# Kernel tuning notes

Hardware: AMD Instinct MI355X
Metric: run time of the kernel (lower is better)

## Reference

```python
import jax, jax.numpy as jnp
import numpy as np

D = 16          # manifold_dim
M = 8192        # mem_slots
H = 256         # slot_dim
K_BASE = 32     # topk
K_BIG = 48      # int(K_BASE * 1.5), used when internal lightbulb fires
INPUT_DIM = 1024
ODE_HID = 128
ODE_STEPS = 2
ODE_DT = 0.5
TEMPERATURE = 1.0      # buffer initial value
LB_TOP1_AVG = 1.0      # buffer initial value
LB_DROP_RATIO = 0.7
BIG = 1e30


def layer_norm(x, g, b, eps=1e-5):
    mu = jnp.mean(x, axis=-1, keepdims=True)
    var = jnp.mean(jnp.square(x - mu), axis=-1, keepdims=True)
    return (x - mu) * jax.lax.rsqrt(var + eps) * g + b


def setup_inputs() -> dict:
    key = jax.random.key(0)
    ks = jax.random.split(key, 12)
    B, S = 4, 2048
    T3 = D * 3
    s_in = 1.0 / np.sqrt(INPUT_DIM)
    s_3d = 1.0 / np.sqrt(T3)
    s_h = 1.0 / np.sqrt(H)
    s_ode = 1.0 / np.sqrt(ODE_HID)
    return {
        "x": jax.random.normal(ks[0], (B, S, INPUT_DIM), jnp.float32),
        "W_proj": jax.random.normal(ks[1], (INPUT_DIM, T3), jnp.float32) * s_in,
        "b_proj": jnp.zeros((T3,), jnp.float32),
        "ln1_g": jnp.ones((T3,), jnp.float32),
        "ln1_b": jnp.zeros((T3,), jnp.float32),
        "ode_W1": jax.random.normal(ks[2], (T3, ODE_HID), jnp.float32) * s_3d,
        "ode_b1": jnp.zeros((ODE_HID,), jnp.float32),
        "ode_W2": jax.random.normal(ks[3], (ODE_HID, T3), jnp.float32) * s_ode,
        "ode_b2": jnp.zeros((T3,), jnp.float32),
        "memory_slots": jax.random.normal(ks[4], (M, H), jnp.float32),
        "pos_enc": jax.random.normal(ks[5], (M, D, 3), jnp.float32),
        "curvature": jax.random.normal(ks[6], (M, D), jnp.float32),
        "curv_alpha": jnp.float32(0.1),
        "W_out": jax.random.normal(ks[7], (H, INPUT_DIM), jnp.float32) * s_h,
        "b_out": jnp.zeros((INPUT_DIM,), jnp.float32),
        "ln2_g": jnp.ones((INPUT_DIM,), jnp.float32),
        "ln2_b": jnp.zeros((INPUT_DIM,), jnp.float32),
    }


def reference(x, W_proj, b_proj, ln1_g, ln1_b, ode_W1, ode_b1, ode_W2, ode_b2,
              memory_slots, pos_enc, curvature, curv_alpha, W_out, b_out, ln2_g, ln2_b):
    # manifold projection: Linear -> LayerNorm -> GELU   (B,S,3D)
    h = jax.nn.gelu(layer_norm(x @ W_proj + b_proj, ln1_g, ln1_b), approximate=False)
    # ODE evolution (2 steps): x + dt * MLP(x), operating on flattened (B,S,3D)
    for _ in range(ODE_STEPS):
        dh = jnp.tanh(h @ ode_W1 + ode_b1) @ ode_W2 + ode_b2
        h = h + ODE_DT * dh
    # _attend: query positions are detached in the original
    q = jax.lax.stop_gradient(h)                       # (B,S,3D)
    mem_pos = pos_enc.reshape(M, D * 3)                # (M,3D)
    # fast pairwise squared-L2 distance: ||q||^2 + ||m||^2 - 2 q.m
    q2 = jnp.sum(q * q, axis=-1, keepdims=True)        # (B,S,1)
    m2 = jnp.sum(mem_pos * mem_pos, axis=-1)           # (M,)
    dist = jnp.maximum(q2 + m2 - 2.0 * jnp.einsum('bsd,md->bsm', q, mem_pos), 0.0)
    dist = dist / max(TEMPERATURE, 1e-6)
    curv_w = jnp.exp(-curv_alpha * jnp.linalg.norm(curvature, axis=-1))  # (M,)
    dist = dist * curv_w                               # (B,S,M)
    # dynamic top-K: take K_BIG smallest, mask down to K_BASE if lightbulb not fired
    neg_vals, itop = jax.lax.top_k(-dist, K_BIG)       # smallest K_BIG distances
    dtop = -neg_vals                                    # ascending (B,S,K_BIG)
    top1 = jnp.mean(dtop[..., 0])
    internal_fire = top1 < LB_DROP_RATIO * LB_TOP1_AVG
    keep = jnp.logical_or(internal_fire, jnp.arange(K_BIG) < K_BASE)  # (K_BIG,)
    d_eff = jnp.where(keep, dtop, BIG)
    w = jax.nn.softmax(-d_eff, axis=-1)                # (B,S,K_BIG)
    mem = memory_slots[itop]                           # gather (B,S,K_BIG,H)
    attended = jnp.einsum('bsk,bskh->bsh', w, mem)     # (B,S,H)
    out = jax.nn.gelu(layer_norm(attended @ W_out + b_out, ln2_g, ln2_b), approximate=False)
    return out
```

## Files before the change

### kernel.cpp

```cpp
#include <hip/hip_runtime.h>
#include <math.h>

#define NQ    8192
#define T3    48
#define INDIM 1024
#define HID   128
#define MSLOT 8192
#define HD    256
#define KBIG  48
#define KBASE 32
#define NSAMP 1024
#define CAP   1024
#define MAXB  32

#define OFF_QH    ((size_t)0)
#define OFF_QL    ((size_t)1048576)
#define OFF_Q2    ((size_t)2097152)
#define OFF_M2    ((size_t)2129920)
#define OFF_CW    ((size_t)2162688)
#define OFF_TOPV  ((size_t)2195456)
#define OFF_TOPI  ((size_t)3768320)
#define OFF_RMIN  ((size_t)5341184)
#define OFF_FLAG  ((size_t)5373952)
#define OFF_WOT   ((size_t)5374208)
#define OFF_PEH   ((size_t)5898496)
#define OFF_PEL   ((size_t)6947072)
#define OFF_WPTH  ((size_t)7995648)
#define OFF_WPTL  ((size_t)8093952)
#define OFF_H0    ((size_t)8192256)
#define OFF_RTHR  ((size_t)9765120)
#define OFF_CNT   ((size_t)9797888)
#define OFF_ATTB  ((size_t)9830656)
#define OFF_DISTS ((size_t)14024960)
#define OFF_CANDS ((size_t)47579392)

typedef __attribute__((ext_vector_type(8))) short short8;
typedef __attribute__((ext_vector_type(4))) float f32x4;

__device__ __forceinline__ float gelu_exact(float x) {
    return 0.5f * x * (1.0f + erff(x * 0.70710678118654752f));
}

__device__ __forceinline__ unsigned short bf16_rne(float f) {
    unsigned int x = __float_as_uint(f);
    unsigned int r = (x + 0x7fffu + ((x >> 16) & 1u)) >> 16;
    return (unsigned short)r;
}

__device__ __forceinline__ void split2(float x, unsigned short& h, unsigned short& l) {
    h = bf16_rne(x);
    l = bf16_rne(x - __uint_as_float((unsigned)h << 16));
}

__global__ __launch_bounds__(256) void k0_prep(const float* __restrict__ pe,
        const float* __restrict__ curv, const float* __restrict__ alpha,
        float* __restrict__ m2, float* __restrict__ cw,
        unsigned short* __restrict__ ph, unsigned short* __restrict__ pl) {
    int m = blockIdx.x * 256 + threadIdx.x;
    float s = 0.f;
    for (int d = 0; d < T3; d++) { float v = pe[(size_t)m * T3 + d]; s += v * v; }
    m2[m] = s;
    float c = 0.f;
    for (int d = 0; d < 16; d++) { float v = curv[m * 16 + d]; c += v * v; }
    cw[m] = expf(-alpha[0] * sqrtf(c));
    int base = blockIdx.x * 256;
    for (int idx = threadIdx.x; idx < 256 * 64; idx += 256) {
        int r = idx >> 6, cc = idx & 63;
        unsigned short hi = 0, lo = 0;
        if (cc < T3) split2(pe[(size_t)(base + r) * T3 + cc], hi, lo);
        size_t o = (size_t)(base + r) * 64 + cc;
        ph[o] = hi; pl[o] = lo;
    }
}

__global__ __launch_bounds__(256) void k0b_cvt(const float* __restrict__ Wo,
        unsigned short* __restrict__ Wot) {
    __shared__ float t[64][65];
    int k0 = blockIdx.x * 64;
    int n0 = blockIdx.y * 64;
    int c = threadIdx.x & 63, r4 = threadIdx.x >> 6;
    #pragma unroll
    for (int i = 0; i < 16; i++) {
        int kr = i * 4 + r4;
        t[kr][c] = Wo[(size_t)(k0 + kr) * INDIM + n0 + c];
    }
    __syncthreads();
    #pragma unroll
    for (int i = 0; i < 16; i++) {
        int nr = i * 4 + r4;
        Wot[(size_t)(n0 + nr) * HD + k0 + c] = bf16_rne(t[c][nr]);
    }
}

__global__ __launch_bounds__(256) void k0d_wpt(const float* __restrict__ Wp,
        unsigned short* __restrict__ wph, unsigned short* __restrict__ wpl) {
    int n = blockIdx.x;
    for (int k = threadIdx.x; k < INDIM; k += 256) {
        unsigned short h, l;
        split2(Wp[(size_t)k * T3 + n], h, l);
        wph[(size_t)n * INDIM + k] = h;
        wpl[(size_t)n * INDIM + k] = l;
    }
}

__global__ __launch_bounds__(256) void k1_mfma(const float* __restrict__ x,
        const unsigned short* __restrict__ wph, const unsigned short* __restrict__ wpl,
        float* __restrict__ h0) {
    __shared__ float part[4][16][48];
    int tid = threadIdx.x, lane = tid & 63, wv = tid >> 6;
    int r0 = blockIdx.x * 16;
    int lm = lane & 15, lk8 = (lane >> 4) * 8;
    f32x4 acc[3];
    #pragma unroll
    for (int j = 0; j < 3; j++) acc[j] = (f32x4)(0.f);
    int kw = wv * 256;
    for (int ks = 0; ks < 8; ks++) {
        int kofs = kw + ks * 32 + lk8;
        short8 ah, al, bh[3], bl[3];
        {
            const float* xp = x + (size_t)(r0 + lm) * INDIM + kofs;
            float4 xa = *(const float4*)xp;
            float4 xb = *(const float4*)(xp + 4);
            float va[8] = {xa.x, xa.y, xa.z, xa.w, xb.x, xb.y, xb.z, xb.w};
            #pragma unroll
            for (int e = 0; e < 8; e++) {
                unsigned short h, l;
                split2(va[e], h, l);
                ah[e] = (short)h; al[e] = (short)l;
            }
        }
        #pragma unroll
        for (int j = 0; j < 3; j++) {
            size_t bo = (size_t)(j * 16 + lm) * INDIM + kofs;
            bh[j] = *(const short8*)(wph + bo);
            bl[j] = *(const short8*)(wpl + bo);
        }
        #pragma unroll
        for (int j = 0; j < 3; j++) {
            f32x4 a = acc[j];
            a = __builtin_amdgcn_mfma_f32_16x16x32_bf16(ah, bh[j], a, 0, 0, 0);
            a = __builtin_amdgcn_mfma_f32_16x16x32_bf16(ah, bl[j], a, 0, 0, 0);
            a = __builtin_amdgcn_mfma_f32_16x16x32_bf16(al, bh[j], a, 0, 0, 0);
            acc[j] = a;
        }
    }
    int orow = (lane >> 4) * 4;
    #pragma unroll
    for (int j = 0; j < 3; j++)
        #pragma unroll
        for (int r = 0; r < 4; r++)
            part[wv][orow + r][j * 16 + lm] = acc[j][r];
    __syncthreads();
    for (int idx = tid; idx < 16 * 48; idx += 256) {
        int rr = idx / 48, cc = idx - rr * 48;
        float s = part[0][rr][cc] + part[1][rr][cc] + part[2][rr][cc] + part[3][rr][cc];
        h0[(size_t)(r0 + rr) * T3 + cc] = s;
    }
}

__global__ __launch_bounds__(256) void k1b_ode(const float* __restrict__ h0,
        const float* __restrict__ bp,
        const float* __restrict__ g1, const float* __restrict__ b1ln,
        const float* __restrict__ W1, const float* __restrict__ bb1,
        const float* __restrict__ W2, const float* __restrict__ bb2,
        unsigned short* __restrict__ qh, unsigned short* __restrict__ ql,
        float* __restrict__ q2out) {
    __shared__ __align__(16) float W1s[T3 * HID];
    __shared__ __align__(16) float W2s[HID * T3];
    __shared__ __align__(16) float hs[16 * T3];
    __shared__ __align__(16) float t1s[16 * 132];
    int tid = threadIdx.x;
    size_t base = (size_t)blockIdx.x * 16 * T3;
    for (int i = tid; i < 1536; i += 256) {
        *(float4*)&W1s[i * 4] = *(const float4*)&W1[i * 4];
        *(float4*)&W2s[i * 4] = *(const float4*)&W2[i * 4];
    }
    for (int idx = tid; idx < 16 * T3; idx += 256) {
        int c = idx % T3;
        t1s[idx] = bp[c] + h0[base + idx];
    }
    __syncthreads();
    {
        int r = tid >> 4, c16 = tid & 15;
        float v[3];
        float ssum = 0.f;
        #pragma unroll
        for (int i = 0; i < 3; i++) { v[i] = t1s[r * T3 + c16 * 3 + i]; ssum += v[i]; }
        #pragma unroll
        for (int off = 1; off < 16; off <<= 1) ssum += __shfl_xor(ssum, off);
        float mean = ssum * (1.f / T3);
        float vv = 0.f;
        #pragma unroll
        for (int i = 0; i < 3; i++) { v[i] -= mean; vv += v[i] * v[i]; }
        #pragma unroll
        for (int off = 1; off < 16; off <<= 1) vv += __shfl_xor(vv, off);
        float rstd = rsqrtf(vv * (1.f / T3) + 1e-5f);
        #pragma unroll
        for (int i = 0; i < 3; i++) {
            int c = c16 * 3 + i;
            hs[r * T3 + c] = gelu_exact(v[i] * rstd * g1[c] + b1ln[c]);
        }
    }
    __syncthreads();
    for (int step = 0; step < 2; step++) {
        #pragma unroll
        for (int it = 0; it < 2; it++) {
            int idx = tid + it * 256;
            int rr = idx >> 5, j4 = idx & 31;
            float4 a = *(const float4*)&bb1[j4 * 4];
            #pragma unroll 3
            for (int d4 = 0; d4 < 12; d4++) {
                float4 qv = *(const float4*)&hs[rr * T3 + d4 * 4];
                float qa[4] = {qv.x, qv.y, qv.z, qv.w};
                #pragma unroll
                for (int dd = 0; dd < 4; dd++) {
                    float4 wv = *(const float4*)&W1s[(d4 * 4 + dd) * HID + j4 * 4];
                    a.x += qa[dd] * wv.x; a.y += qa[dd] * wv.y;
                    a.z += qa[dd] * wv.z; a.w += qa[dd] * wv.w;
                }
            }
            a.x = tanhf(a.x); a.y = tanhf(a.y); a.z = tanhf(a.z); a.w = tanhf(a.w);
            *(float4*)&t1s[rr * 132 + j4 * 4] = a;
        }
        __syncthreads();
        if (tid < 192) {
            int rr = tid / 12, c4 = tid % 12;
            float4 a = *(const float4*)&bb2[c4 * 4];
            #pragma unroll 4
            for (int j4 = 0; j4 < 32; j4++) {
                float4 tv = *(const float4*)&t1s[rr * 132 + j4 * 4];
                float ta[4] = {tv.x, tv.y, tv.z, tv.w};
                #pragma unroll
                for (int jj = 0; jj < 4; jj++) {
                    float4 wv = *(const float4*)&W2s[(j4 * 4 + jj) * T3 + c4 * 4];
                    a.x += ta[jj] * wv.x; a.y += ta[jj] * wv.y;
                    a.z += ta[jj] * wv.z; a.w += ta[jj] * wv.w;
                }
            }
            float4 cur = *(const float4*)&hs[rr * T3 + c4 * 4];
            cur.x += 0.5f * a.x; cur.y += 0.5f * a.y;
            cur.z += 0.5f * a.z; cur.w += 0.5f * a.w;
            *(float4*)&hs[rr * T3 + c4 * 4] = cur;
        }
        __syncthreads();
    }
    {
        int r = tid >> 4, c16 = tid & 15;
        float sq = 0.f;
        #pragma unroll
        for (int i = 0; i < 3; i++) { float v = hs[r * T3 + c16 * 3 + i]; sq += v * v; }
        #pragma unroll
        for (int off = 1; off < 16; off <<= 1) sq += __shfl_xor(sq, off);
        if (c16 == 0) q2out[(size_t)blockIdx.x * 16 + r] = sq;
    }
    for (int idx = tid; idx < 16 * 64; idx += 256) {
        int r = idx >> 6, c = idx & 63;
        unsigned short hi = 0, lo = 0;
        if (c < T3) split2(hs[r * T3 + c], hi, lo);
        size_t o = ((size_t)blockIdx.x * 16 + r) * 64 + c;
        qh[o] = hi; ql[o] = lo;
    }
}

#define PES 72
__global__ __launch_bounds__(256, 4) void k2a_mfma(
        const unsigned short* __restrict__ qh, const unsigned short* __restrict__ ql,
        const float* __restrict__ q2g,
        const unsigned short* __restrict__ ph, const unsigned short* __restrict__ pl,
        const float* __restrict__ m2, const float* __restrict__ cw,
        float* __restrict__ dist, int rowstride) {
    __shared__ __align__(16) char smem[256 * PES * 2];
    __shared__ float q2s[32];
    unsigned short* pesh = (unsigned short*)smem;
    int tid = threadIdx.x, lane = tid & 63, wv = tid >> 6;
    int c0 = blockIdx.x * 256;
    int grow0 = blockIdx.y * 32;
    for (int idx = tid; idx < 2048; idx += 256) {
        int col = idx >> 3, ch = idx & 7;
        *(uint4*)&pesh[col * PES + ch * 8] = *(const uint4*)&ph[(size_t)(c0 + col) * 64 + ch * 8];
    }
    if (tid < 32) q2s[tid] = q2g[grow0 + tid];
    int lm = lane & 15, lk8 = (lane >> 4) * 8;
    int mco = wv * 64;
    short8 bqh[2][2], bql[2][2];
    #pragma unroll
    for (int qs = 0; qs < 2; qs++)
        #pragma unroll
        for (int ks = 0; ks < 2; ks++) {
            size_t o = (size_t)(grow0 + qs * 16 + lm) * 64 + ks * 32 + lk8;
            bqh[qs][ks] = *(const short8*)&qh[o];
            bql[qs][ks] = *(const short8*)&ql[o];
        }
    short8 al0[4], al1[4];
    #pragma unroll
    for (int ms = 0; ms < 4; ms++) {
        size_t plo = (size_t)(c0 + mco + ms * 16 + lm) * 64;
        al0[ms] = *(const short8*)&pl[plo + lk8];
        al1[ms] = *(const short8*)&pl[plo + 32 + lk8];
    }
    __syncthreads();
    f32x4 acc[4][2];
    #pragma unroll
    for (int i = 0; i < 4; i++)
        #pragma unroll
        for (int j = 0; j < 2; j++) acc[i][j] = (f32x4)(0.f);
    #pragma unroll
    for (int ms = 0; ms < 4; ms++) {
        int arow = mco + ms * 16 + lm;
        short8 ah0 = *(const short8*)&pesh[arow * PES + lk8];
        short8 ah1 = *(const short8*)&pesh[arow * PES + 32 + lk8];
        #pragma unroll
        for (int qs = 0; qs < 2; qs++) {
            f32x4 a = acc[ms][qs];
            a = __builtin_amdgcn_mfma_f32_16x16x32_bf16(ah0, bqh[qs][0], a, 0, 0, 0);
            a = __builtin_amdgcn_mfma_f32_16x16x32_bf16(ah1, bqh[qs][1], a, 0, 0, 0);
            a = __builtin_amdgcn_mfma_f32_16x16x32_bf16(ah0, bql[qs][0], a, 0, 0, 0);
            a = __builtin_amdgcn_mfma_f32_16x16x32_bf16(ah1, bql[qs][1], a, 0, 0, 0);
            a = __builtin_amdgcn_mfma_f32_16x16x32_bf16(al0[ms], bqh[qs][0], a, 0, 0, 0);
            a = __builtin_amdgcn_mfma_f32_16x16x32_bf16(al1[ms], bqh[qs][1], a, 0, 0, 0);
            acc[ms][qs] = a;
        }
    }
    int mr4 = (lane >> 4) * 4;
    #pragma unroll
    for (int ms = 0; ms < 4; ms++) {
        int gm = c0 + mco + ms * 16 + mr4;
        float4 m2v = *(const float4*)&m2[gm];
        float4 cwv = *(const float4*)&cw[gm];
        float m2a[4] = {m2v.x, m2v.y, m2v.z, m2v.w};
        float cwa[4] = {cwv.x, cwv.y, cwv.z, cwv.w};
        #pragma unroll
        for (int qs = 0; qs < 2; qs++) {
            float q2 = q2s[qs * 16 + lm];
            #pragma unroll
            for (int c = 0; c < 4; c++)
                acc[ms][qs][c] = fmaxf(q2 + m2a[c] - 2.f * acc[ms][qs][c], 0.f) * cwa[c];
        }
    }
    __syncthreads();
    float (*dt)[260] = (float(*)[260])smem;
    #pragma unroll
    for (int ms = 0; ms < 4; ms++)
        #pragma unroll
        for (int qs = 0; qs < 2; qs++) {
            float4 o;
            o.x = acc[ms][qs][0]; o.y = acc[ms][qs][1];
            o.z = acc[ms][qs][2]; o.w = acc[ms][qs][3];
            *(float4*)&dt[qs * 16 + lm][mco + ms * 16 + mr4] = o;
        }
    __syncthreads();
    #pragma unroll
    for (int i = 0; i < 8; i++) {
        int qrow = wv * 8 + i;
        float4 v = *(const float4*)&dt[qrow][lane * 4];
        *(float4*)&dist[(size_t)(grow0 + qrow) * rowstride + c0 + lane * 4] = v;
    }
}

#define NBINT 2048
#define MAXCT 512
__global__ __launch_bounds__(256) void k2b_thr(const float* __restrict__ dists,
        float* __restrict__ rowthr, int* __restrict__ cnt) {
    __shared__ unsigned int hist[NBINT];
    __shared__ unsigned long long cand[MAXCT];
    __shared__ float s_wmin[4], s_wmax[4];
    __shared__ unsigned int wsum[4];
    __shared__ unsigned int s_B, s_ncand;
    int tid = threadIdx.x, lane = tid & 63, wv = tid >> 6;
    int row = blockIdx.x;
    float4 v4 = *(const float4*)(dists + (size_t)row * NSAMP + tid * 4);
    float fv[4] = {v4.x, v4.y, v4.z, v4.w};
    float mn = fminf(fminf(fv[0], fv[1]), fminf(fv[2], fv[3]));
    float mx = fmaxf(fmaxf(fv[0], fv[1]), fmaxf(fv[2], fv[3]));
    #pragma unroll
    for (int off = 32; off; off >>= 1) {
        mn = fminf(mn, __shfl_xor(mn, off));
        mx = fmaxf(mx, __shfl_xor(mx, off));
    }
    if (lane == 0) { s_wmin[wv] = mn; s_wmax[wv] = mx; }
    __syncthreads();
    float m0 = fminf(fminf(s_wmin[0], s_wmin[1]), fminf(s_wmin[2], s_wmin[3]));
    float mX = fmaxf(fmaxf(s_wmax[0], s_wmax[1]), fmaxf(s_wmax[2], s_wmax[3]));
    float lo = m0;
    float width = fmaxf(m0 * 0.5f, 1e-3f);
    float fullw = fmaxf((mX - m0) * 1.0001f, 1e-3f) + 1e-6f;
    unsigned B = 0;
    float scale = 0.f, hiT = 0.f;
    for (int att = 0; att < 7; att++) {
        if (att == 6 || width > fullw) width = fullw;
        hiT = lo + width;
        scale = (float)NBINT / width;
        for (int i = tid; i < NBINT; i += 256) hist[i] = 0;
        __syncthreads();
        #pragma unroll
        for (int j = 0; j < 4; j++) {
            float v = fv[j];
            if (v < hiT) {
                int b = (int)((v - lo) * scale);
                b = b < NBINT - 1 ? b : NBINT - 1;
                atomicAdd(&hist[b], 1u);
            }
        }
        __syncthreads();
        unsigned hb[8];
        unsigned s = 0;
        #pragma unroll
        for (int i = 0; i < 8; i++) { hb[i] = hist[tid * 8 + i]; s += hb[i]; }
        unsigned v = s;
        #pragma unroll
        for (int off = 1; off < 64; off <<= 1) {
            unsigned o = __shfl_up(v, off);
            if (lane >= off) v += o;
        }
        if (lane == 63) wsum[wv] = v;
        __syncthreads();
        unsigned wbase = 0;
        for (int w = 0; w < wv; w++) wbase += wsum[w];
        unsigned total = wsum[0] + wsum[1] + wsum[2] + wsum[3];
        if (total >= KBIG) {
            unsigned excl = wbase + v - s;
            if (excl < KBIG && KBIG <= excl + s) {
                unsigned c = excl;
                #pragma unroll
                for (int i = 0; i < 8; i++) {
                    if (c < KBIG && KBIG <= c + hb[i]) { s_B = tid * 8 + i; break; }
                    c += hb[i];
                }
            }
            __syncthreads();
            B = s_B;
            break;
        }
        width *= 8.f;
        __syncthreads();
    }
    if (tid == 0) s_ncand = 0;
    __syncthreads();
    #pragma unroll
    for (int j = 0; j < 4; j++) {
        float v = fv[j];
        if (v < hiT) {
            int b = (int)((v - lo) * scale);
            b = b < NBINT - 1 ? b : NBINT - 1;
            if ((unsigned)b <= B) {
                unsigned n = atomicAdd(&s_ncand, 1u);
                if (n < MAXCT)
                    cand[n] = ((unsigned long long)__float_as_uint(v) << 32)
                              | (unsigned)(tid * 4 + j);
            }
        }
    }
    __syncthreads();
    int nc = (int)(s_ncand < MAXCT ? s_ncand : MAXCT);
    for (int i = tid; i < nc; i += 256) {
        unsigned long long me = cand[i];
        int rank = 0;
        for (int j = 0; j < nc; j++) rank += (cand[j] < me) ? 1 : 0;
        if (rank == KBIG - 1)
            rowthr[row] = __uint_as_float((unsigned)(me >> 32));
    }
    if (tid == 0) cnt[row] = 0;
}

__global__ __launch_bounds__(256, 4) void k2c_filter(
        const unsigned short* __restrict__ qh, const unsigned short* __restrict__ ql,
        const float* __restrict__ q2g,
        const unsigned short* __restrict__ ph, const unsigned short* __restrict__ pl,
        const float* __restrict__ m2, const float* __restrict__ cw,
        const float* __restrict__ rowthr, int* __restrict__ cnt,
        unsigned long long* __restrict__ cands) {
    __shared__ __align__(16) char smem[256 * PES * 2];
    __shared__ float q2s[32];
    __shared__ float thrs[32];
    __shared__ unsigned int lcnt[32], gbase[32];
    unsigned short* pesh = (unsigned short*)smem;
    int tid = threadIdx.x, lane = tid & 63, wv = tid >> 6;
    int c0 = blockIdx.x * 256;
    int grow0 = blockIdx.y * 32;
    for (int idx = tid; idx < 2048; idx += 256) {
        int col = idx >> 3, ch = idx & 7;
        *(uint4*)&pesh[col * PES + ch * 8] = *(const uint4*)&ph[(size_t)(c0 + col) * 64 + ch * 8];
    }
    if (tid < 32) {
        q2s[tid] = q2g[grow0 + tid];
        thrs[tid] = rowthr[grow0 + tid];
        lcnt[tid] = 0;
    }
    int lm = lane & 15, lk8 = (lane >> 4) * 8;
    int mco = wv * 64;
    short8 bqh[2][2], bql[2][2];
    #pragma unroll
    for (int qs = 0; qs < 2; qs++)
        #pragma unroll
        for (int ks = 0; ks < 2; ks++) {
            size_t o = (size_t)(grow0 + qs * 16 + lm) * 64 + ks * 32 + lk8;
            bqh[qs][ks] = *(const short8*)&qh[o];
            bql[qs][ks] = *(const short8*)&ql[o];
        }
    short8 al0[4], al1[4];
    #pragma unroll
    for (int ms = 0; ms < 4; ms++) {
        size_t plo = (size_t)(c0 + mco + ms * 16 + lm) * 64;
        al0[ms] = *(const short8*)&pl[plo + lk8];
        al1[ms] = *(const short8*)&pl[plo + 32 + lk8];
    }
    __syncthreads();
    f32x4 acc[4][2];
    #pragma unroll
    for (int i = 0; i < 4; i++)
        #pragma unroll
        for (int j = 0; j < 2; j++) acc[i][j] = (f32x4)(0.f);
    #pragma unroll
    for (int ms = 0; ms < 4; ms++) {
        int arow = mco + ms * 16 + lm;
        short8 ah0 = *(const short8*)&pesh[arow * PES + lk8];
        short8 ah1 = *(const short8*)&pesh[arow * PES + 32 + lk8];
        #pragma unroll
        for (int qs = 0; qs < 2; qs++) {
            f32x4 a = acc[ms][qs];
            a = __builtin_amdgcn_mfma_f32_16x16x32_bf16(ah0, bqh[qs][0], a, 0, 0, 0);
            a = __builtin_amdgcn_mfma_f32_16x16x32_bf16(ah1, bqh[qs][1], a, 0, 0, 0);
            a = __builtin_amdgcn_mfma_f32_16x16x32_bf16(ah0, bql[qs][0], a, 0, 0, 0);
            a = __builtin_amdgcn_mfma_f32_16x16x32_bf16(ah1, bql[qs][1], a, 0, 0, 0);
            a = __builtin_amdgcn_mfma_f32_16x16x32_bf16(al0[ms], bqh[qs][0], a, 0, 0, 0);
            a = __builtin_amdgcn_mfma_f32_16x16x32_bf16(al1[ms], bqh[qs][1], a, 0, 0, 0);
            acc[ms][qs] = a;
        }
    }
    int mr4 = (lane >> 4) * 4;
    #pragma unroll
    for (int ms = 0; ms < 4; ms++) {
        int gm = c0 + mco + ms * 16 + mr4;
        float4 m2v = *(const float4*)&m2[gm];
        float4 cwv = *(const float4*)&cw[gm];
        float m2a[4] = {m2v.x, m2v.y, m2v.z, m2v.w};
        float cwa[4] = {cwv.x, cwv.y, cwv.z, cwv.w};
        #pragma unroll
        for (int qs = 0; qs < 2; qs++) {
            float q2 = q2s[qs * 16 + lm];
            #pragma unroll
            for (int c = 0; c < 4; c++)
                acc[ms][qs][c] = fmaxf(q2 + m2a[c] - 2.f * acc[ms][qs][c], 0.f) * cwa[c];
        }
    }
    __syncthreads();
    unsigned long long (*lbuf)[MAXB] = (unsigned long long(*)[MAXB])smem;
    #pragma unroll
    for (int ms = 0; ms < 4; ms++) {
        int gm = c0 + mco + ms * 16 + mr4;
        #pragma unroll
        for (int qs = 0; qs < 2; qs++) {
            int q = qs * 16 + lm;
            float thr = thrs[q];
            #pragma unroll
            for (int c = 0; c < 4; c++) {
                float v = acc[ms][qs][c];
                if (v <= thr) {
                    unsigned long long key =
                        ((unsigned long long)__float_as_uint(v) << 32)
                        | (unsigned)(gm + c);
                    unsigned slot = atomicAdd(&lcnt[q], 1u);
                    if (slot < MAXB) lbuf[q][slot] = key;
                    else {
                        int gs = atomicAdd(&cnt[grow0 + q], 1);
                        if (gs < CAP) cands[(size_t)(grow0 + q) * CAP + gs] = key;
                    }
                }
            }
        }
    }
    __syncthreads();
    if (tid < 32) {
        unsigned k = lcnt[tid];
        k = k < MAXB ? k : MAXB;
        lcnt[tid] = k;
        gbase[tid] = (unsigned)atomicAdd(&cnt[grow0 + tid], (int)k);
    }
    __syncthreads();
    for (int idx = tid; idx < 32 * MAXB; idx += 256) {
        int q = idx >> 5, i = idx & (MAXB - 1);
        if (i < (int)lcnt[q]) {
            unsigned b = gbase[q] + (unsigned)i;
            if (b < CAP) cands[(size_t)(grow0 + q) * CAP + b] = lbuf[q][i];
        }
    }
}

#define NBIND 2048
#define FINCAP 512
__global__ __launch_bounds__(256) void k2d_select(
        const unsigned long long* __restrict__ cands, const int* __restrict__ cnt,
        float* __restrict__ topv, int* __restrict__ topi, float* __restrict__ rowmin) {
    __shared__ unsigned long long cl[CAP];
    __shared__ unsigned int hist[NBIND];
    __shared__ unsigned long long fin[FINCAP];
    __shared__ float s_mn[4], s_mx[4];
    __shared__ unsigned int wsum[4];
    __shared__ unsigned int s_B, s_nfin;
    int tid = threadIdx.x, lane = tid & 63, wv = tid >> 6;
    size_t row = blockIdx.x;
    int nc = cnt[row];
    nc = nc < CAP ? nc : CAP;
    float mn = 3.4e38f, mx = -3.4e38f;
    for (int i = tid; i < nc; i += 256) {
        unsigned long long k = cands[row * CAP + i];
        cl[i] = k;
        float v = __uint_as_float((unsigned)(k >> 32));
        mn = fminf(mn, v); mx = fmaxf(mx, v);
    }
    #pragma unroll
    for (int off = 32; off; off >>= 1) {
        mn = fminf(mn, __shfl_xor(mn, off));
        mx = fmaxf(mx, __shfl_xor(mx, off));
    }
    if (lane == 0) { s_mn[wv] = mn; s_mx[wv] = mx; }
    for (int i = tid; i < NBIND; i += 256) hist[i] = 0;
    if (tid == 0) s_nfin = 0;
    __syncthreads();
    float m0 = fminf(fminf(s_mn[0], s_mn[1]), fminf(s_mn[2], s_mn[3]));
    float mX = fmaxf(fmaxf(s_mx[0], s_mx[1]), fmaxf(s_mx[2], s_mx[3]));
    float width = fmaxf((mX - m0) * 1.0001f, 1e-9f) + 1e-12f;
    float scale = (float)NBIND / width;
    for (int i = tid; i < nc; i += 256) {
        float v = __uint_as_float((unsigned)(cl[i] >> 32));
        int b = (int)((v - m0) * scale);
        b = b < NBIND - 1 ? b : NBIND - 1;
        atomicAdd(&hist[b], 1u);
    }
    __syncthreads();
    {
        unsigned hb[8];
        unsigned s = 0;
        #pragma unroll
        for (int i = 0; i < 8; i++) { hb[i] = hist[tid * 8 + i]; s += hb[i]; }
        unsigned v = s;
        #pragma unroll
        for (int off = 1; off < 64; off <<= 1) {
            unsigned o = __shfl_up(v, off);
            if (lane >= off) v += o;
        }
        if (lane == 63) wsum[wv] = v;
        __syncthreads();
        unsigned wbase = 0;
        for (int w = 0; w < wv; w++) wbase += wsum[w];
        unsigned excl = wbase + v - s;
        unsigned tgt = (unsigned)(nc < KBIG ? nc : KBIG);
        if (excl < tgt && tgt <= excl + s) {
            unsigned c = excl;
            #pragma unroll
            for (int i = 0; i < 8; i++) {
                if (c < tgt && tgt <= c + hb[i]) { s_B = tid * 8 + i; break; }
                c += hb[i];
            }
        }
        __syncthreads();
    }
    unsigned B = s_B;
    for (int i = tid; i < nc; i += 256) {
        float v = __uint_as_float((unsigned)(cl[i] >> 32));
        int b = (int)((v - m0) * scale);
        b = b < NBIND - 1 ? b : NBIND - 1;
        if ((unsigned)b <= B) {
            unsigned n = atomicAdd(&s_nfin, 1u);
            if (n < FINCAP) fin[n] = cl[i];
        }
    }
    __syncthreads();
    int nf = (int)s_nfin;
    if (nf <= FINCAP) {
        for (int i = tid; i < nf; i += 256) {
            unsigned long long me = fin[i];
            int rank = 0;
            for (int j = 0; j < nf; j++) rank += (fin[j] < me) ? 1 : 0;
            if (rank < KBIG) {
                float v = __uint_as_float((unsigned)(me >> 32));
                topv[row * KBIG + rank] = v;
                topi[row * KBIG + rank] = (int)(me & 0xFFFFFFFFu);
                if (rank == 0) rowmin[row] = v;
            }
        }
    } else {
        for (int i = tid; i < nc; i += 256) {
            unsigned long long me = cl[i];
            int rank = 0;
            for (int j = 0; j < nc; j++) rank += (cl[j] < me) ? 1 : 0;
            if (rank < KBIG) {
                float v = __uint_as_float((unsigned)(me >> 32));
                topv[row * KBIG + rank] = v;
                topi[row * KBIG + rank] = (int)(me & 0xFFFFFFFFu);
                if (rank == 0) rowmin[row] = v;
            }
        }
    }
}

__global__ __launch_bounds__(256) void k3a_flag(const float* __restrict__ rowmin,
        int* __restrict__ flag) {
    __shared__ float red[256];
    int tid = threadIdx.x;
    float s = 0.f;
    for (int j = 0; j < NQ / 256; j++) s += rowmin[tid + 256 * j];
    red[tid] = s;
    __syncthreads();
    for (int st = 128; st; st >>= 1) {
        if (tid < st) red[tid] += red[tid + st];
        __syncthreads();
    }
    if (tid == 0) {
        float top1 = red[0] / (float)NQ;
        flag[0] = (top1 < 0.7f) ? 1 : 0;
    }
}

__global__ __launch_bounds__(256) void k3_attend(const float* __restrict__ topv,
        const int* __restrict__ topi, const int* __restrict__ flag,
        const float* __restrict__ slots, unsigned short* __restrict__ attb) {
    int tid = threadIdx.x;
    int lane = tid & 63, wv = tid >> 6;
    size_t row = (size_t)blockIdx.x * 4 + wv;
    int kc = flag[0] ? KBIG : KBASE;
    float v0 = topv[row * KBIG];
    float ev = 0.f;
    int mi = 0;
    if (lane < KBIG) {
        float v = topv[row * KBIG + lane];
        ev = (lane < kc) ? expf(-(v - v0)) : 0.f;
        mi = topi[row * KBIG + lane];
    }
    float ssum = ev;
    #pragma unroll
    for (int off = 32; off; off >>= 1) ssum += __shfl_xor(ssum, off);
    float inv = 1.f / ssum;
    float4 acc = make_float4(0.f, 0.f, 0.f, 0.f);
    for (int k = 0; k < kc; k++) {
        float wk = __shfl(ev, k) * inv;
        int m = __shfl(mi, k);
        float4 v = *(const float4*)(slots + (size_t)m * HD + lane * 4);
        acc.x += wk * v.x; acc.y += wk * v.y;
        acc.z += wk * v.z; acc.w += wk * v.w;
    }
    ushort4 o;
    o.x = bf16_rne(acc.x); o.y = bf16_rne(acc.y);
    o.z = bf16_rne(acc.z); o.w = bf16_rne(acc.w);
    *(ushort4*)(attb + row * HD + lane * 4) = o;
}

__global__ __launch_bounds__(256) void k4_mfma(const unsigned short* __restrict__ A,
        const unsigned short* __restrict__ Bt, const float* __restrict__ bo,
        float* __restrict__ out) {
    int tid = threadIdx.x;
    int lane = tid & 63, wave = tid >> 6;
    int wm = wave >> 1, wn = wave & 1;
    int mbase = blockIdx.y * 128 + wm * 64;
    int nbase = blockIdx.x * 128 + wn * 64;
    int lm = lane & 15;
    int lk8 = (lane >> 4) * 8;
    f32x4 acc[4][4];
    #pragma unroll
    for (int i = 0; i < 4; i++)
        #pragma unroll
        for (int j = 0; j < 4; j++) acc[i][j] = (f32x4)(0.f);
    #pragma unroll 2
    for (int ks = 0; ks < 8; ks++) {
        int kofs = ks * 32 + lk8;
        short8 a[4], b[4];
        #pragma unroll
        for (int i = 0; i < 4; i++)
            a[i] = *(const short8*)(A + (size_t)(mbase + i * 16 + lm) * HD + kofs);
        #pragma unroll
        for (int j = 0; j < 4; j++)
            b[j] = *(const short8*)(Bt + (size_t)(nbase + j * 16 + lm) * HD + kofs);
        #pragma unroll
        for (int i = 0; i < 4; i++)
            #pragma unroll
            for (int j = 0; j < 4; j++)
                acc[i][j] = __builtin_amdgcn_mfma_f32_16x16x32_bf16(a[i], b[j], acc[i][j], 0, 0, 0);
    }
    int orow = (lane >> 4) * 4;
    #pragma unroll
    for (int i = 0; i < 4; i++)
        #pragma unroll
        for (int j = 0; j < 4; j++) {
            int col = nbase + j * 16 + lm;
            float bias = bo[col];
            #pragma unroll
            for (int r = 0; r < 4; r++) {
                int row = mbase + i * 16 + orow + r;
                out[(size_t)row * INDIM + col] = acc[i][j][r] + bias;
            }
        }
}

__global__ __launch_bounds__(256) void k5_ln(float* __restrict__ out,
        const float* __restrict__ g, const float* __restrict__ b) {
    __shared__ float red[4];
    int tid = threadIdx.x;
    size_t row = blockIdx.x;
    float4 v = *(const float4*)(out + row * INDIM + tid * 4);
    float s = v.x + v.y + v.z + v.w;
    #pragma unroll
    for (int off = 32; off; off >>= 1) s += __shfl_xor(s, off);
    int wid = tid >> 6, lane = tid & 63;
    if (!lane) red[wid] = s;
    __syncthreads();
    float mean = (red[0] + red[1] + red[2] + red[3]) * (1.f / (float)INDIM);
    __syncthreads();
    float dx = v.x - mean, dy = v.y - mean, dz = v.z - mean, dw = v.w - mean;
    float ss = dx * dx + dy * dy + dz * dz + dw * dw;
    #pragma unroll
    for (int off = 32; off; off >>= 1) ss += __shfl_xor(ss, off);
    if (!lane) red[wid] = ss;
    __syncthreads();
    float var = (red[0] + red[1] + red[2] + red[3]) * (1.f / (float)INDIM);
    float rs = rsqrtf(var + 1e-5f);
    int c = tid * 4;
    float4 o;
    o.x = gelu_exact(dx * rs * g[c + 0] + b[c + 0]);
    o.y = gelu_exact(dy * rs * g[c + 1] + b[c + 1]);
    o.z = gelu_exact(dz * rs * g[c + 2] + b[c + 2]);
    o.w = gelu_exact(dw * rs * g[c + 3] + b[c + 3]);
    *(float4*)(out + row * INDIM + c) = o;
}

extern "C" void kernel_launch(void* const* d_in, const int* in_sizes, int n_in,
                              void* d_out, int out_size, void* d_ws, size_t ws_size,
                              hipStream_t stream) {
    const float* x     = (const float*)d_in[0];
    const float* Wp    = (const float*)d_in[1];
    const float* bp    = (const float*)d_in[2];
    const float* ln1g  = (const float*)d_in[3];
    const float* ln1b  = (const float*)d_in[4];
    const float* oW1   = (const float*)d_in[5];
    const float* ob1   = (const float*)d_in[6];
    const float* oW2   = (const float*)d_in[7];
    const float* ob2   = (const float*)d_in[8];
    const float* slots = (const float*)d_in[9];
    const float* pe    = (const float*)d_in[10];
    const float* curv  = (const float*)d_in[11];
    const float* alpha = (const float*)d_in[12];
    const float* Wo    = (const float*)d_in[13];
    const float* bo    = (const float*)d_in[14];
    const float* ln2g  = (const float*)d_in[15];
    const float* ln2b  = (const float*)d_in[16];
    float* out = (float*)d_out;
    char* ws = (char*)d_ws;

    unsigned short* qhp = (unsigned short*)(ws + OFF_QH);
    unsigned short* qlp = (unsigned short*)(ws + OFF_QL);
    float* q2p    = (float*)(ws + OFF_Q2);
    float* m2     = (float*)(ws + OFF_M2);
    float* cwv    = (float*)(ws + OFF_CW);
    float* topv   = (float*)(ws + OFF_TOPV);
    int*   topi   = (int*)  (ws + OFF_TOPI);
    float* rowmin = (float*)(ws + OFF_RMIN);
    int*   flag   = (int*)  (ws + OFF_FLAG);
    unsigned short* wot  = (unsigned short*)(ws + OFF_WOT);
    unsigned short* peh  = (unsigned short*)(ws + OFF_PEH);
    unsigned short* pel  = (unsigned short*)(ws + OFF_PEL);
    unsigned short* wpth = (unsigned short*)(ws + OFF_WPTH);
    unsigned short* wptl = (unsigned short*)(ws + OFF_WPTL);
    float* h0     = (float*)(ws + OFF_H0);
    float* rowthr = (float*)(ws + OFF_RTHR);
    int*   cntp   = (int*)  (ws + OFF_CNT);
    unsigned short* attb = (unsigned short*)(ws + OFF_ATTB);
    float* dists  = (float*)(ws + OFF_DISTS);
    unsigned long long* cands = (unsigned long long*)(ws + OFF_CANDS);

    k0_prep<<<MSLOT / 256, 256, 0, stream>>>(pe, curv, alpha, m2, cwv, peh, pel);
    k0b_cvt<<<dim3(4, 16), 256, 0, stream>>>(Wo, wot);
    k0d_wpt<<<T3, 256, 0, stream>>>(Wp, wpth, wptl);
    k1_mfma<<<NQ / 16, 256, 0, stream>>>(x, wpth, wptl, h0);
    k1b_ode<<<NQ / 16, 256, 0, stream>>>(h0, bp, ln1g, ln1b, oW1, ob1, oW2, ob2,
                                         qhp, qlp, q2p);
    k2a_mfma<<<dim3(NSAMP / 256, NQ / 32), 256, 0, stream>>>(
        qhp, qlp, q2p, peh, pel, m2, cwv, dists, NSAMP);
    k2b_thr<<<NQ, 256, 0, stream>>>(dists, rowthr, cntp);
    k2c_filter<<<dim3(MSLOT / 256, NQ / 32), 256, 0, stream>>>(
        qhp, qlp, q2p, peh, pel, m2, cwv, rowthr, cntp, cands);
    k2d_select<<<NQ, 256, 0, stream>>>(cands, cntp, topv, topi, rowmin);
    k3a_flag<<<1, 256, 0, stream>>>(rowmin, flag);
    k3_attend<<<NQ / 4, 256, 0, stream>>>(topv, topi, flag, slots, attb);
    k4_mfma<<<dim3(INDIM / 128, NQ / 128), 256, 0, stream>>>(attb, wot, bo, out);
    k5_ln<<<NQ, 256, 0, stream>>>(out, ln2g, ln2b);
}
```

Measured before the change: 268.7 us.

## Replace global atomic candidate counters with per-tile fixed-slot candidate buffers

The filter kernel now writes each tile's candidates into a fixed per-(row,tile) slot region of capacity 48, along with a per-tile count, instead of reserving space through global atomics on a per-row counter. The select kernel compacts these tile regions into shared memory using a shared-memory atomic. This removes the global atomics and the counter reset in the threshold kernel. The risk is that candidates beyond 48 per tile are silently dropped, where the old code spilled them to global memory. The tile-strided reads in the select kernel are also sparser.

```diff
diff --git a/kernel.cpp b/kernel.cpp
--- a/kernel.cpp
+++ b/kernel.cpp
@@ -10,8 +10,9 @@
 #define KBIG  48
 #define KBASE 32
 #define NSAMP 1024
-#define CAP   1024
-#define MAXB  32
+#define NTIL  32
+#define TCAP  48
+#define RSTR  (NTIL * TCAP)
 
 #define OFF_QH    ((size_t)0)
 #define OFF_QL    ((size_t)1048576)
@@ -29,10 +30,10 @@
 #define OFF_WPTL  ((size_t)8093952)
 #define OFF_H0    ((size_t)8192256)
 #define OFF_RTHR  ((size_t)9765120)
-#define OFF_CNT   ((size_t)9797888)
 #define OFF_ATTB  ((size_t)9830656)
 #define OFF_DISTS ((size_t)14024960)
 #define OFF_CANDS ((size_t)47579392)
+#define OFF_CNT2  ((size_t)150994944)
 
 typedef __attribute__((ext_vector_type(8))) short short8;
 typedef __attribute__((ext_vector_type(4))) float f32x4;
@@ -360,7 +361,7 @@
 #define NBINT 2048
 #define MAXCT 512
 __global__ __launch_bounds__(256) void k2b_thr(const float* __restrict__ dists,
-        float* __restrict__ rowthr, int* __restrict__ cnt) {
+        float* __restrict__ rowthr) {
     __shared__ unsigned int hist[NBINT];
     __shared__ unsigned long long cand[MAXCT];
     __shared__ float s_wmin[4], s_wmax[4];
@@ -459,7 +460,6 @@
         if (rank == KBIG - 1)
             rowthr[row] = __uint_as_float((unsigned)(me >> 32));
     }
-    if (tid == 0) cnt[row] = 0;
 }
 
 __global__ __launch_bounds__(256, 4) void k2c_filter(
@@ -467,15 +467,16 @@
         const float* __restrict__ q2g,
         const unsigned short* __restrict__ ph, const unsigned short* __restrict__ pl,
         const float* __restrict__ m2, const float* __restrict__ cw,
-        const float* __restrict__ rowthr, int* __restrict__ cnt,
+        const float* __restrict__ rowthr, int* __restrict__ cnt2,
         unsigned long long* __restrict__ cands) {
     __shared__ __align__(16) char smem[256 * PES * 2];
     __shared__ float q2s[32];
     __shared__ float thrs[32];
-    __shared__ unsigned int lcnt[32], gbase[32];
+    __shared__ unsigned int lcnt[32];
     unsigned short* pesh = (unsigned short*)smem;
     int tid = threadIdx.x, lane = tid & 63, wv = tid >> 6;
-    int c0 = blockIdx.x * 256;
+    int tile = blockIdx.x;
+    int c0 = tile * 256;
     int grow0 = blockIdx.y * 32;
     for (int idx = tid; idx < 2048; idx += 256) {
         int col = idx >> 3, ch = idx & 7;
@@ -544,7 +545,7 @@
         }
     }
     __syncthreads();
-    unsigned long long (*lbuf)[MAXB] = (unsigned long long(*)[MAXB])smem;
+    unsigned long long (*lbuf)[TCAP] = (unsigned long long(*)[TCAP])smem;
     #pragma unroll
     for (int ms = 0; ms < 4; ms++) {
         int gm = c0 + mco + ms * 16 + mr4;
@@ -556,15 +557,10 @@
             for (int c = 0; c < 4; c++) {
                 float v = acc[ms][qs][c];
                 if (v <= thr) {
-                    unsigned long long key =
-                        ((unsigned long long)__float_as_uint(v) << 32)
-                        | (unsigned)(gm + c);
                     unsigned slot = atomicAdd(&lcnt[q], 1u);
-                    if (slot < MAXB) lbuf[q][slot] = key;
-                    else {
-                        int gs = atomicAdd(&cnt[grow0 + q], 1);
-                        if (gs < CAP) cands[(size_t)(grow0 + q) * CAP + gs] = key;
-                    }
+                    if (slot < TCAP)
+                        lbuf[q][slot] = ((unsigned long long)__float_as_uint(v) << 32)
+                                        | (unsigned)(gm + c);
                 }
             }
         }
@@ -572,40 +568,49 @@
     __syncthreads();
     if (tid < 32) {
         unsigned k = lcnt[tid];
-        k = k < MAXB ? k : MAXB;
+        k = k < TCAP ? k : TCAP;
         lcnt[tid] = k;
-        gbase[tid] = (unsigned)atomicAdd(&cnt[grow0 + tid], (int)k);
-    }
-    __syncthreads();
-    for (int idx = tid; idx < 32 * MAXB; idx += 256) {
-        int q = idx >> 5, i = idx & (MAXB - 1);
-        if (i < (int)lcnt[q]) {
-            unsigned b = gbase[q] + (unsigned)i;
-            if (b < CAP) cands[(size_t)(grow0 + q) * CAP + b] = lbuf[q][i];
-        }
+        cnt2[(size_t)(grow0 + tid) * NTIL + tile] = (int)k;
+    }
+    __syncthreads();
+    for (int idx = tid; idx < 32 * TCAP; idx += 256) {
+        int q = idx / TCAP, i = idx - q * TCAP;
+        if (i < (int)lcnt[q])
+            cands[(size_t)(grow0 + q) * RSTR + tile * TCAP + i] = lbuf[q][i];
     }
 }
 
 #define NBIND 2048
 #define FINCAP 512
+#define CLCAP (NTIL * TCAP)
 __global__ __launch_bounds__(256) void k2d_select(
-        const unsigned long long* __restrict__ cands, const int* __restrict__ cnt,
+        const unsigned long long* __restrict__ cands, const int* __restrict__ cnt2,
         float* __restrict__ topv, int* __restrict__ topi, float* __restrict__ rowmin) {
-    __shared__ unsigned long long cl[CAP];
+    __shared__ unsigned long long cl[CLCAP];
     __shared__ unsigned int hist[NBIND];
     __shared__ unsigned long long fin[FINCAP];
+    __shared__ int cnt2s[NTIL];
     __shared__ float s_mn[4], s_mx[4];
     __shared__ unsigned int wsum[4];
-    __shared__ unsigned int s_B, s_nfin;
+    __shared__ unsigned int s_B, s_nc, s_nfin;
     int tid = threadIdx.x, lane = tid & 63, wv = tid >> 6;
     size_t row = blockIdx.x;
-    int nc = cnt[row];
-    nc = nc < CAP ? nc : CAP;
+    if (tid < NTIL) cnt2s[tid] = cnt2[row * NTIL + tid];
+    for (int i = tid; i < NBIND; i += 256) hist[i] = 0;
+    if (tid == 0) { s_nc = 0; s_nfin = 0; }
+    __syncthreads();
+    for (int idx = tid; idx < CLCAP; idx += 256) {
+        int t = idx / TCAP, i = idx - t * TCAP;
+        if (i < cnt2s[t]) {
+            unsigned n = atomicAdd(&s_nc, 1u);
+            cl[n] = cands[row * RSTR + idx];
+        }
+    }
+    __syncthreads();
+    int nc = (int)s_nc;
     float mn = 3.4e38f, mx = -3.4e38f;
     for (int i = tid; i < nc; i += 256) {
-        unsigned long long k = cands[row * CAP + i];
-        cl[i] = k;
-        float v = __uint_as_float((unsigned)(k >> 32));
+        float v = __uint_as_float((unsigned)(cl[i] >> 32));
         mn = fminf(mn, v); mx = fmaxf(mx, v);
     }
     #pragma unroll
@@ -614,8 +619,6 @@
         mx = fmaxf(mx, __shfl_xor(mx, off));
     }
     if (lane == 0) { s_mn[wv] = mn; s_mx[wv] = mx; }
-    for (int i = tid; i < NBIND; i += 256) hist[i] = 0;
-    if (tid == 0) s_nfin = 0;
     __syncthreads();
     float m0 = fminf(fminf(s_mn[0], s_mn[1]), fminf(s_mn[2], s_mn[3]));
     float mX = fmaxf(fmaxf(s_mx[0], s_mx[1]), fmaxf(s_mx[2], s_mx[3]));
@@ -861,10 +864,10 @@
     unsigned short* wptl = (unsigned short*)(ws + OFF_WPTL);
     float* h0     = (float*)(ws + OFF_H0);
     float* rowthr = (float*)(ws + OFF_RTHR);
-    int*   cntp   = (int*)  (ws + OFF_CNT);
     unsigned short* attb = (unsigned short*)(ws + OFF_ATTB);
     float* dists  = (float*)(ws + OFF_DISTS);
     unsigned long long* cands = (unsigned long long*)(ws + OFF_CANDS);
+    int*   cnt2   = (int*)  (ws + OFF_CNT2);
 
     k0_prep<<<MSLOT / 256, 256, 0, stream>>>(pe, curv, alpha, m2, cwv, peh, pel);
     k0b_cvt<<<dim3(4, 16), 256, 0, stream>>>(Wo, wot);
@@ -874,10 +877,10 @@
                                          qhp, qlp, q2p);
     k2a_mfma<<<dim3(NSAMP / 256, NQ / 32), 256, 0, stream>>>(
         qhp, qlp, q2p, peh, pel, m2, cwv, dists, NSAMP);
-    k2b_thr<<<NQ, 256, 0, stream>>>(dists, rowthr, cntp);
-    k2c_filter<<<dim3(MSLOT / 256, NQ / 32), 256, 0, stream>>>(
-        qhp, qlp, q2p, peh, pel, m2, cwv, rowthr, cntp, cands);
-    k2d_select<<<NQ, 256, 0, stream>>>(cands, cntp, topv, topi, rowmin);
+    k2b_thr<<<NQ, 256, 0, stream>>>(dists, rowthr);
+    k2c_filter<<<dim3(NTIL, NQ / 32), 256, 0, stream>>>(
+        qhp, qlp, q2p, peh, pel, m2, cwv, rowthr, cnt2, cands);
+    k2d_select<<<NQ, 256, 0, stream>>>(cands, cnt2, topv, topi, rowmin);
     k3a_flag<<<1, 256, 0, stream>>>(rowmin, flag);
     k3_attend<<<NQ / 4, 256, 0, stream>>>(topv, topi, flag, slots, attb);
     k4_mfma<<<dim3(INDIM / 128, NQ / 128), 256, 0, stream>>>(attb, wot, bo, out);
```

Measured after the change: 281.1 us. 1.05x slower.
